# Kernel optimization log

Hardware: AMD Instinct MI355X
Metric: run time of the kernel (lower is better)

Reference implementation:

```python
import jax, jax.numpy as jnp
import numpy as np

IN_FEATURES = 2048
OUT_FEATURES = 2048
TOP_K = 1024


def setup_inputs() -> dict:
    key = jax.random.key(0)
    kx, kw, kb = jax.random.split(key, 3)
    bound = 1.0 / np.sqrt(IN_FEATURES)
    x = jax.random.normal(kx, (8, 2048, IN_FEATURES), dtype=jnp.float32)
    weight = jax.random.uniform(kw, (OUT_FEATURES, IN_FEATURES), dtype=jnp.float32,
                                minval=-bound, maxval=bound)
    bias = jax.random.uniform(kb, (OUT_FEATURES,), dtype=jnp.float32,
                              minval=-bound, maxval=bound)
    return {"x": x, "weight": weight, "bias": bias}


def _topk_mask(weight: jnp.ndarray, k: int) -> jnp.ndarray:
    # Per output row, keep the k largest-magnitude weights (binary mask).
    _, idx = jax.lax.top_k(jnp.abs(weight), k)            # [out, k]
    rows = jnp.arange(weight.shape[0])[:, None]            # [out, 1]
    mask = jnp.zeros_like(weight).at[rows, idx].set(1.0)   # scatter ones
    return mask


def reference(x, weight, bias):
    # y = x @ (mask * W)^T + b, mask = top-k by |W| per output feature
    mask = _topk_mask(weight, TOP_K)
    masked_weight = weight * mask                          # [out, in]
    return jnp.einsum('bsi,oi->bso', x, masked_weight) + bias
```

## Files before the change

### kernel.cpp

```cpp
#include <hip/hip_runtime.h>

typedef __attribute__((ext_vector_type(8))) short s16x8;
typedef __attribute__((ext_vector_type(4))) float f32x4;
typedef __attribute__((ext_vector_type(8))) unsigned short u16x8;

#define GLB(p) ((const __attribute__((address_space(1))) void*)(p))
#define LDS(p) ((__attribute__((address_space(3))) void*)(p))

#define BAR() __builtin_amdgcn_s_barrier()
#define VMC(n) asm volatile("s_waitcnt vmcnt(" #n ")" ::: "memory")

__device__ __forceinline__ unsigned short f2bf(float f) {
  unsigned u = __float_as_uint(f);
  u += 0x7fffu + ((u >> 16) & 1u);
  return (unsigned short)(u >> 16);
}

__global__ __launch_bounds__(256) void prep_kernel(
    const float* __restrict__ W, unsigned short* __restrict__ Wb,
    const float* __restrict__ X, unsigned short* __restrict__ Xb) {
  __shared__ int hist[4096];
  __shared__ int scanres[2];
  __shared__ int wsum[4];
  const int tid  = threadIdx.x;

  if (blockIdx.x >= 2048) {
    const size_t i = ((size_t)(blockIdx.x - 2048) * 256 + tid) * 8;
    const float4* xp = (const float4*)(X + i);
    const float4 a = xp[0], b = xp[1];
    u16x8 o;
    o[0] = f2bf(a.x); o[1] = f2bf(a.y); o[2] = f2bf(a.z); o[3] = f2bf(a.w);
    o[4] = f2bf(b.x); o[5] = f2bf(b.y); o[6] = f2bf(b.z); o[7] = f2bf(b.w);
    *(u16x8*)(Xb + i) = o;
    return;
  }

  const int lane = tid & 63;
  const int wv   = tid >> 6;
  const int row  = blockIdx.x;
  const float* wr = W + (size_t)row * 2048;

  const float4 v0 = *(const float4*)(wr + tid * 8);
  const float4 v1 = *(const float4*)(wr + tid * 8 + 4);
  float val[8] = {v0.x, v0.y, v0.z, v0.w, v1.x, v1.y, v1.z, v1.w};
  unsigned key[8];
#pragma unroll
  for (int e = 0; e < 8; ++e) key[e] = __float_as_uint(val[e]) & 0x7fffffffu;

  unsigned prefix = 0;
  int rem = 1024;

  for (int i = tid; i < 4096; i += 256) hist[i] = 0;
  __syncthreads();
#pragma unroll
  for (int e = 0; e < 8; ++e) atomicAdd(&hist[key[e] >> 20], 1);
  __syncthreads();
  if (wv == 0) {
    const int base = 4096 - (lane + 1) * 64;
    int s = 0;
    for (int b = 0; b < 64; ++b) s += hist[base + b];
    int cum = s;
#pragma unroll
    for (int off = 1; off < 64; off <<= 1) {
      int o = __shfl_up(cum, off, 64);
      if (lane >= off) cum += o;
    }
    const int cumex = cum - s;
    if (cumex < rem && rem <= cum) {
      int running = cumex;
      for (int b = 63; b >= 0; --b) {
        int h = hist[base + b];
        if (running + h >= rem) { scanres[0] = base + b; scanres[1] = rem - running; break; }
        running += h;
      }
    }
  }
  __syncthreads();
  prefix = ((unsigned)scanres[0]) << 20;
  rem = scanres[1];
  __syncthreads();

  for (int i = tid; i < 1024; i += 256) hist[i] = 0;
  __syncthreads();
#pragma unroll
  for (int e = 0; e < 8; ++e)
    if ((key[e] >> 20) == (prefix >> 20)) atomicAdd(&hist[(key[e] >> 10) & 1023], 1);
  __syncthreads();
  if (wv == 0) {
    const int base = 1024 - (lane + 1) * 16;
    int s = 0;
    for (int b = 0; b < 16; ++b) s += hist[base + b];
    int cum = s;
#pragma unroll
    for (int off = 1; off < 64; off <<= 1) {
      int o = __shfl_up(cum, off, 64);
      if (lane >= off) cum += o;
    }
    const int cumex = cum - s;
    if (cumex < rem && rem <= cum) {
      int running = cumex;
      for (int b = 15; b >= 0; --b) {
        int h = hist[base + b];
        if (running + h >= rem) { scanres[0] = base + b; scanres[1] = rem - running; break; }
        running += h;
      }
    }
  }
  __syncthreads();
  prefix |= ((unsigned)scanres[0]) << 10;
  rem = scanres[1];
  __syncthreads();

  for (int i = tid; i < 1024; i += 256) hist[i] = 0;
  __syncthreads();
#pragma unroll
  for (int e = 0; e < 8; ++e)
    if ((key[e] >> 10) == (prefix >> 10)) atomicAdd(&hist[key[e] & 1023], 1);
  __syncthreads();
  if (wv == 0) {
    const int base = 1024 - (lane + 1) * 16;
    int s = 0;
    for (int b = 0; b < 16; ++b) s += hist[base + b];
    int cum = s;
#pragma unroll
    for (int off = 1; off < 64; off <<= 1) {
      int o = __shfl_up(cum, off, 64);
      if (lane >= off) cum += o;
    }
    const int cumex = cum - s;
    if (cumex < rem && rem <= cum) {
      int running = cumex;
      for (int b = 15; b >= 0; --b) {
        int h = hist[base + b];
        if (running + h >= rem) { scanres[0] = base + b; scanres[1] = rem - running; break; }
        running += h;
      }
    }
  }
  __syncthreads();
  const unsigned T = prefix | (unsigned)scanres[0];
  rem = scanres[1];

  int eqcnt = 0;
#pragma unroll
  for (int e = 0; e < 8; ++e) eqcnt += (key[e] == T) ? 1 : 0;
  int c = eqcnt;
#pragma unroll
  for (int off = 1; off < 64; off <<= 1) {
    int o = __shfl_up(c, off, 64);
    if (lane >= off) c += o;
  }
  if (lane == 63) wsum[wv] = c;
  __syncthreads();
  int wavebase = 0;
  for (int j = 0; j < wv; ++j) wavebase += wsum[j];
  const int myex = wavebase + c - eqcnt;

  u16x8 o;
  int r = 0;
#pragma unroll
  for (int e = 0; e < 8; ++e) {
    const bool iseq = (key[e] == T);
    const bool keep = (key[e] > T) || (iseq && (myex + r) < rem);
    r += iseq ? 1 : 0;
    o[e] = keep ? f2bf(val[e]) : (unsigned short)0;
  }
  *(u16x8*)(Wb + (size_t)row * 2048 + tid * 8) = o;
}

__global__ __launch_bounds__(512, 2) void gemm_bt_kernel(
    const unsigned short* __restrict__ A,
    const unsigned short* __restrict__ B,
    const float* __restrict__ bias,
    float* __restrict__ C) {
  constexpr int K = 2048;
  constexpr int N = 2048;
  constexpr int T = K / 64;
  constexpr size_t HK = (size_t)128 * K;

  __shared__ __align__(16) char lds_[131072];

  const int tid = threadIdx.x;
  const int l   = tid & 63;
  const int wv  = tid >> 6;
  const int wm  = wv & 1;
  const int wn  = wv >> 1;

  const int lin = blockIdx.x;
  const int o   = (lin & 7) * 64 + (lin >> 3);
  const int tm  = o >> 3;
  const int tn  = o & 7;

  int rS[2], cS[2];
#pragma unroll
  for (int e = 0; e < 2; ++e) {
    const int d   = (e * 512 + tid) * 16;
    const int off = d ^ (((d >> 9) & 1) << 5);
    rS[e] = ((off >> 11) << 4) | ((off >> 6) & 15);
    cS[e] = (((off >> 10) & 1) << 5) | (((off >> 4) & 3) << 3);
  }
  const unsigned short* const pA0 = A + (size_t)(tm * 256 + rS[0]) * K + cS[0];
  const unsigned short* const pA1 = A + (size_t)(tm * 256 + rS[1]) * K + cS[1];
  const unsigned short* const pB0 = B + (size_t)(tn * 256 + rS[0]) * K + cS[0];
  const unsigned short* const pB1 = B + (size_t)(tn * 256 + rS[1]) * K + cS[1];

  auto stage = [&](const unsigned short* g0, const unsigned short* g1, char* d) {
    __builtin_amdgcn_global_load_lds(GLB(g0), LDS(d + wv * 1024), 16, 0, 0);
    __builtin_amdgcn_global_load_lds(GLB(g1), LDS(d + 8192 + wv * 1024), 16, 0, 0);
  };

  const int laneoff = (((l & 15) << 6) | ((l >> 4) << 4)) ^ ((l & 8) << 2);
  const char* const aRd = (const char*)lds_ + wm * 2048 + laneoff;
  const char* const bRd = (const char*)lds_ + 65536 + wn * 2048 + laneoff;

  f32x4 acc[8][4] = {};

  stage(pA0,            pA1,            lds_);
  stage(pB0 + HK,       pB1 + HK,       lds_ + 65536 + 16384);
  stage(pA0 + HK,       pA1 + HK,       lds_ + 16384);
  stage(pB0,            pB1,            lds_ + 65536);
  stage(pA0 + 64,       pA1 + 64,       lds_ + 32768);
  stage(pB0 + HK + 64,  pB1 + HK + 64,  lds_ + 65536 + 32768 + 16384);
  stage(pA0 + HK + 64,  pA1 + HK + 64,  lds_ + 32768 + 16384);
  VMC(6);
  BAR();

  for (int t = 0; t < T; ++t) {
    const int bb = t & 1;
    const char* aT = aRd + bb * 32768;
    const char* bT = bRd + bb * 32768;
    char* sA  = lds_ + bb * 32768;
    char* sB  = lds_ + 65536 + bb * 32768;
    char* sBn = lds_ + 65536 + (bb ^ 1) * 32768;

    s16x8 af[4][2], bLo[2][2], bHi[2][2];

    if (t + 1 < T)
      stage(pB0 + (size_t)(t + 1) * 64, pB1 + (size_t)(t + 1) * 64, sBn);
#pragma unroll
    for (int i = 0; i < 4; ++i)
      af[i][0] = *(const s16x8*)(aT + i * 4096);
#pragma unroll
    for (int j = 0; j < 2; ++j)
      bLo[j][0] = *(const s16x8*)(bT + j * 8192);
#pragma unroll
    for (int i = 0; i < 4; ++i)
      af[i][1] = *(const s16x8*)(aT + i * 4096 + 1024);
#pragma unroll
    for (int j = 0; j < 2; ++j)
      bLo[j][1] = *(const s16x8*)(bT + j * 8192 + 1024);
#pragma unroll
    for (int j = 0; j < 2; ++j) {
      bHi[j][0] = *(const s16x8*)(bT + 16384 + j * 8192);
      bHi[j][1] = *(const s16x8*)(bT + 16384 + j * 8192 + 1024);
    }
    __builtin_amdgcn_s_setprio(1);
#pragma unroll
    for (int kk = 0; kk < 2; ++kk)
#pragma unroll
      for (int i = 0; i < 4; ++i)
#pragma unroll
        for (int j = 0; j < 2; ++j)
          acc[i][j] = __builtin_amdgcn_mfma_f32_16x16x32_bf16(af[i][kk], bLo[j][kk], acc[i][j], 0, 0, 0);
    __builtin_amdgcn_s_setprio(0);
    BAR();

    if (t + 2 < T)
      stage(pA0 + (size_t)(t + 2) * 64, pA1 + (size_t)(t + 2) * 64, sA);
    __builtin_amdgcn_s_setprio(1);
#pragma unroll
    for (int kk = 0; kk < 2; ++kk)
#pragma unroll
      for (int i = 0; i < 4; ++i)
#pragma unroll
        for (int j = 0; j < 2; ++j)
          acc[i][j + 2] = __builtin_amdgcn_mfma_f32_16x16x32_bf16(af[i][kk], bHi[j][kk], acc[i][j + 2], 0, 0, 0);
    __builtin_amdgcn_s_setprio(0);
#pragma unroll
    for (int i = 0; i < 4; ++i) {
      af[i][0] = *(const s16x8*)(aT + 16384 + i * 4096);
      af[i][1] = *(const s16x8*)(aT + 16384 + i * 4096 + 1024);
    }
    BAR();

    if (t + 2 < T)
      stage(pB0 + HK + (size_t)(t + 2) * 64, pB1 + HK + (size_t)(t + 2) * 64, sB + 16384);
    __builtin_amdgcn_s_setprio(1);
#pragma unroll
    for (int kk = 0; kk < 2; ++kk)
#pragma unroll
      for (int i = 0; i < 4; ++i)
#pragma unroll
        for (int j = 0; j < 2; ++j)
          acc[i + 4][j + 2] = __builtin_amdgcn_mfma_f32_16x16x32_bf16(af[i][kk], bHi[j][kk], acc[i + 4][j + 2], 0, 0, 0);
    __builtin_amdgcn_s_setprio(0);
#pragma unroll
    for (int j = 0; j < 2; ++j) {
      bLo[j][0] = *(const s16x8*)(bT + j * 8192);
      bLo[j][1] = *(const s16x8*)(bT + j * 8192 + 1024);
    }
    BAR();

    if (t + 2 < T)
      stage(pA0 + HK + (size_t)(t + 2) * 64, pA1 + HK + (size_t)(t + 2) * 64, sA + 16384);
    __builtin_amdgcn_s_setprio(1);
#pragma unroll
    for (int kk = 0; kk < 2; ++kk)
#pragma unroll
      for (int i = 0; i < 4; ++i)
#pragma unroll
        for (int j = 0; j < 2; ++j)
          acc[i + 4][j] = __builtin_amdgcn_mfma_f32_16x16x32_bf16(af[i][kk], bLo[j][kk], acc[i + 4][j], 0, 0, 0);
    __builtin_amdgcn_s_setprio(0);
    if (t + 2 < T) { VMC(6); } else { VMC(0); }
    BAR();
  }

  float bv[4];
#pragma unroll
  for (int j = 0; j < 4; ++j)
    bv[j] = bias[tn * 256 + (4 * j + wn) * 16 + (l & 15)];

  const int crow0 = tm * 256 + wm * 16 + (l >> 4) * 4;
  const int ccol0 = tn * 256 + wn * 16 + (l & 15);
  float* Cp = C + (size_t)crow0 * N + ccol0;
#pragma unroll
  for (int i = 0; i < 8; ++i)
#pragma unroll
    for (int j = 0; j < 4; ++j)
#pragma unroll
      for (int r = 0; r < 4; ++r)
        Cp[(size_t)(i * 32 + r) * N + j * 64] = acc[i][j][r] + bv[j];
}

extern "C" void kernel_launch(void* const* d_in, const int* in_sizes, int n_in,
                              void* d_out, int out_size, void* d_ws, size_t ws_size,
                              hipStream_t stream) {
  const float* x    = (const float*)d_in[0];
  const float* w    = (const float*)d_in[1];
  const float* bias = (const float*)d_in[2];
  float* out = (float*)d_out;

  constexpr int M = 8 * 2048;
  constexpr int N = 2048;
  constexpr int K = 2048;

  unsigned short* xb = (unsigned short*)d_ws;
  unsigned short* wb = xb + (size_t)M * K;

  const int conv_blocks = ((size_t)M * K) / (256 * 8);
  prep_kernel<<<2048 + conv_blocks, 256, 0, stream>>>(w, wb, x, xb);
  gemm_bt_kernel<<<(M / 256) * (N / 256), 512, 0, stream>>>(xb, wb, bias, out);
}
```

Measured before the change: 351.4 us.

## Replace staggered quarter-tile prefetch with simple whole-tile double buffering

The GEMM main loop previously issued prefetches for quarter-tiles of A and B, two iterations ahead and interleaved with the MFMA phases, separated by three intra-iteration barriers. It now prefetches the entire next K-tile into the opposite buffer at the start of each iteration, keeps bLo in registers instead of reloading it, and uses one full vmcnt(0) wait and one barrier per iteration. This cuts barrier count and register reloads, but global-load latency is now hidden by only one iteration of compute and the loads are issued in a single burst.

Result: no change. 352.6 us (+0.3%).

```diff
diff --git a/kernel.cpp b/kernel.cpp
--- a/kernel.cpp
+++ b/kernel.cpp
@@ -215,28 +215,30 @@
 
   f32x4 acc[8][4] = {};
 
-  stage(pA0,            pA1,            lds_);
-  stage(pB0 + HK,       pB1 + HK,       lds_ + 65536 + 16384);
-  stage(pA0 + HK,       pA1 + HK,       lds_ + 16384);
-  stage(pB0,            pB1,            lds_ + 65536);
-  stage(pA0 + 64,       pA1 + 64,       lds_ + 32768);
-  stage(pB0 + HK + 64,  pB1 + HK + 64,  lds_ + 65536 + 32768 + 16384);
-  stage(pA0 + HK + 64,  pA1 + HK + 64,  lds_ + 32768 + 16384);
-  VMC(6);
+  stage(pA0,      pA1,      lds_);
+  stage(pA0 + HK, pA1 + HK, lds_ + 16384);
+  stage(pB0,      pB1,      lds_ + 65536);
+  stage(pB0 + HK, pB1 + HK, lds_ + 65536 + 16384);
+  VMC(0);
   BAR();
 
   for (int t = 0; t < T; ++t) {
     const int bb = t & 1;
     const char* aT = aRd + bb * 32768;
     const char* bT = bRd + bb * 32768;
-    char* sA  = lds_ + bb * 32768;
-    char* sB  = lds_ + 65536 + bb * 32768;
-    char* sBn = lds_ + 65536 + (bb ^ 1) * 32768;
+    char* nA = lds_ + (bb ^ 1) * 32768;
+    char* nB = lds_ + 65536 + (bb ^ 1) * 32768;
+
+    if (t + 1 < T) {
+      const size_t ko = (size_t)(t + 1) * 64;
+      stage(pA0 + ko,      pA1 + ko,      nA);
+      stage(pA0 + HK + ko, pA1 + HK + ko, nA + 16384);
+      stage(pB0 + ko,      pB1 + ko,      nB);
+      stage(pB0 + HK + ko, pB1 + HK + ko, nB + 16384);
+    }
 
     s16x8 af[4][2], bLo[2][2], bHi[2][2];
 
-    if (t + 1 < T)
-      stage(pB0 + (size_t)(t + 1) * 64, pB1 + (size_t)(t + 1) * 64, sBn);
 #pragma unroll
     for (int i = 0; i < 4; ++i)
       af[i][0] = *(const s16x8*)(aT + i * 4096);
@@ -254,6 +256,7 @@
       bHi[j][0] = *(const s16x8*)(bT + 16384 + j * 8192);
       bHi[j][1] = *(const s16x8*)(bT + 16384 + j * 8192 + 1024);
     }
+
     __builtin_amdgcn_s_setprio(1);
 #pragma unroll
     for (int kk = 0; kk < 2; ++kk)
@@ -263,10 +266,7 @@
         for (int j = 0; j < 2; ++j)
           acc[i][j] = __builtin_amdgcn_mfma_f32_16x16x32_bf16(af[i][kk], bLo[j][kk], acc[i][j], 0, 0, 0);
     __builtin_amdgcn_s_setprio(0);
-    BAR();
-
-    if (t + 2 < T)
-      stage(pA0 + (size_t)(t + 2) * 64, pA1 + (size_t)(t + 2) * 64, sA);
+
     __builtin_amdgcn_s_setprio(1);
 #pragma unroll
     for (int kk = 0; kk < 2; ++kk)
@@ -276,15 +276,13 @@
         for (int j = 0; j < 2; ++j)
           acc[i][j + 2] = __builtin_amdgcn_mfma_f32_16x16x32_bf16(af[i][kk], bHi[j][kk], acc[i][j + 2], 0, 0, 0);
     __builtin_amdgcn_s_setprio(0);
+
 #pragma unroll
     for (int i = 0; i < 4; ++i) {
       af[i][0] = *(const s16x8*)(aT + 16384 + i * 4096);
       af[i][1] = *(const s16x8*)(aT + 16384 + i * 4096 + 1024);
     }
-    BAR();
-
-    if (t + 2 < T)
-      stage(pB0 + HK + (size_t)(t + 2) * 64, pB1 + HK + (size_t)(t + 2) * 64, sB + 16384);
+
     __builtin_amdgcn_s_setprio(1);
 #pragma unroll
     for (int kk = 0; kk < 2; ++kk)
@@ -294,15 +292,7 @@
         for (int j = 0; j < 2; ++j)
           acc[i + 4][j + 2] = __builtin_amdgcn_mfma_f32_16x16x32_bf16(af[i][kk], bHi[j][kk], acc[i + 4][j + 2], 0, 0, 0);
     __builtin_amdgcn_s_setprio(0);
-#pragma unroll
-    for (int j = 0; j < 2; ++j) {
-      bLo[j][0] = *(const s16x8*)(bT + j * 8192);
-      bLo[j][1] = *(const s16x8*)(bT + j * 8192 + 1024);
-    }
-    BAR();
-
-    if (t + 2 < T)
-      stage(pA0 + HK + (size_t)(t + 2) * 64, pA1 + HK + (size_t)(t + 2) * 64, sA + 16384);
+
     __builtin_amdgcn_s_setprio(1);
 #pragma unroll
     for (int kk = 0; kk < 2; ++kk)
@@ -312,7 +302,8 @@
         for (int j = 0; j < 2; ++j)
           acc[i + 4][j] = __builtin_amdgcn_mfma_f32_16x16x32_bf16(af[i][kk], bLo[j][kk], acc[i + 4][j], 0, 0, 0);
     __builtin_amdgcn_s_setprio(0);
-    if (t + 2 < T) { VMC(6); } else { VMC(0); }
+
+    VMC(0);
     BAR();
   }
 
```
